# Optimization experiments

Measured on AMD Instinct MI355X. Metric: run time of the kernel, lower is better.

Reference implementation:

```python
import jax, jax.numpy as jnp
import numpy as np

D = 256   # feature_dim
NQ = 512  # num query keypoints
NK = 512  # num key/value keypoints


def setup_inputs() -> dict:
    key = jax.random.key(0)
    ks = jax.random.split(key, 10)
    def w(k, shape, fan_in):
        return jax.random.normal(k, shape, dtype=jnp.float32) / np.sqrt(fan_in)
    inp = {
        "x": jax.random.normal(ks[0], (1, D, NQ), dtype=jnp.float32),
        "source": jax.random.normal(ks[1], (1, D, NK), dtype=jnp.float32),
        # MLPAttention score MLP: Conv1d(2D->D,k=1), ReLU, Conv1d(D->1,k=1)
        "w1": w(ks[2], (D, 2 * D), 2 * D),
        "b1": w(ks[3], (D,), 2 * D),
        "w2": w(ks[4], (1, D), D),
        "b2": w(ks[5], (1,), D),
        # outer MLP: Conv1d(2D->2D,k=1), ReLU, Conv1d(2D->D,k=1) with zero bias init
        "wa": w(ks[6], (2 * D, 2 * D), 2 * D),
        "ba": w(ks[7], (2 * D,), 2 * D),
        "wb": w(ks[8], (D, 2 * D), 2 * D),
        "bb": jnp.zeros((D,), dtype=jnp.float32),
    }
    return inp


def reference(x, source, w1, b1, w2, b2, wa, ba, wb, bb):
    d = x.shape[1]
    q = x[0]       # [D, nq]
    k = source[0]  # [D, nk]
    # cat((q broadcast over nk, k broadcast over nq)) then Conv1d(2D->D) is
    # equivalent to splitting w1 into query/key halves and broadcasting:
    w1q, w1k = w1[:, :d], w1[:, d:]
    aq = w1q @ q + b1[:, None]                       # [D, nq]
    ak = w1k @ k                                     # [D, nk]
    h = jax.nn.relu(aq[:, :, None] + ak[:, None, :])  # [D, nq, nk]
    scores = (jnp.einsum('d,dnm->nm', w2[0], h) + b2[0])[None]  # [1, nq, nk]
    prob = jax.nn.softmax(scores, axis=-1)
    message = jnp.einsum('bnm,bdm->bdn', prob, source)  # [1, D, nq]
    # outer MLP on cat([x, message], channel dim)
    cat = jnp.concatenate([x, message], axis=1)         # [1, 2D, nq]
    h2 = jax.nn.relu(jnp.einsum('oc,bcn->bon', wa, cat) + ba[None, :, None])
    y = jnp.einsum('oc,bcn->bon', wb, h2) + bb[None, :, None]  # [1, D, nq]
    return (y, scores)
```

## Files before the change

### kernel.cpp

```cpp
#include <hip/hip_runtime.h>
#include <hip/hip_bf16.h>

#define DD 256
#define NN 512

typedef __attribute__((ext_vector_type(8))) short short8;
typedef __attribute__((ext_vector_type(4))) float floatx4;

__device__ __forceinline__ unsigned short f2bf(float f) {
  unsigned u = __float_as_uint(f);
  u += 0x7FFFu + ((u >> 16) & 1u);
  return (unsigned short)(u >> 16);
}

__device__ __forceinline__ short8 ldfrag(const unsigned short* __restrict__ base,
                                         int row, int ld, int k, int lane) {
  const unsigned short* p = base + (row + (lane & 15)) * ld + k + ((lane >> 4) << 3);
  return *(const short8*)p;
}

__device__ __forceinline__ void gemm_acc(floatx4 acc[4],
    const unsigned short* __restrict__ A, int lda,
    const unsigned short* __restrict__ BT, int ldb,
    int K, int a_k0, int b_k0, int m0, int n0, int lane) {
  for (int k = 0; k < K; k += 32) {
    short8 a = ldfrag(A, m0, lda, a_k0 + k, lane);
#pragma unroll
    for (int nf = 0; nf < 4; ++nf) {
      short8 b = ldfrag(BT, n0 + nf * 16, ldb, b_k0 + k, lane);
      acc[nf] = __builtin_amdgcn_mfma_f32_16x16x32_bf16(a, b, acc[nf], 0, 0, 0);
    }
  }
}

template <bool COLBIAS, bool ROWBIAS, bool RELU, bool OUTBF>
__device__ __forceinline__ void gemm_epi(floatx4 acc[4],
    const float* __restrict__ bias, void* __restrict__ C, int ldc,
    int m0, int n0, int lane) {
  const int col = lane & 15;
  const int q = lane >> 4;
#pragma unroll
  for (int nf = 0; nf < 4; ++nf) {
    const int n = n0 + nf * 16 + col;
    const float cb = COLBIAS ? bias[n] : 0.0f;
#pragma unroll
    for (int r = 0; r < 4; ++r) {
      const int m = m0 + q * 4 + r;
      float v = acc[nf][r] + cb + (ROWBIAS ? bias[m] : 0.0f);
      if (RELU) v = fmaxf(v, 0.0f);
      if (OUTBF) ((unsigned short*)C)[m * ldc + n] = f2bf(v);
      else       ((float*)C)[m * ldc + n] = v;
    }
  }
}

__device__ __forceinline__ void acc_zero(floatx4 acc[4]) {
#pragma unroll
  for (int i = 0; i < 4; ++i) {
    acc[i][0] = 0.f; acc[i][1] = 0.f; acc[i][2] = 0.f; acc[i][3] = 0.f;
  }
}

__global__ __launch_bounds__(256) void prep_kernel(
    const float* __restrict__ x, const float* __restrict__ src,
    const float* __restrict__ w1, const float* __restrict__ wa,
    const float* __restrict__ wb,
    unsigned short* __restrict__ w1b, unsigned short* __restrict__ wab,
    unsigned short* __restrict__ wbb, unsigned short* __restrict__ srcb,
    unsigned short* __restrict__ xT, unsigned short* __restrict__ srcT) {
  const int bid = blockIdx.x;
  const int tid = threadIdx.x;
  if (bid < 640) {
    const float* in; unsigned short* out; int off;
    if (bid < 128)      { in = w1;  out = w1b; off = bid; }
    else if (bid < 384) { in = wa;  out = wab; off = bid - 128; }
    else if (bid < 512) { in = wb;  out = wbb; off = bid - 384; }
    else                { in = src; out = srcb; off = bid - 512; }
    const int i = off * 1024 + tid * 4;
    const float4 v = *(const float4*)(in + i);
    const unsigned lo = (unsigned)f2bf(v.x) | ((unsigned)f2bf(v.y) << 16);
    const unsigned hi = (unsigned)f2bf(v.z) | ((unsigned)f2bf(v.w) << 16);
    *(uint2*)(out + i) = make_uint2(lo, hi);
  } else {
    __shared__ float tile[32][33];
    const int b = bid - 640;
    const float* in = (b >> 7) ? src : x;
    unsigned short* out = (b >> 7) ? srcT : xT;
    const int t = b & 127;
    const int n0 = (t >> 3) * 32;
    const int d0 = (t & 7) * 32;
    const int tx = tid & 31, ty = tid >> 5;
#pragma unroll
    for (int i = ty; i < 32; i += 8)
      tile[i][tx] = in[(d0 + i) * NN + n0 + tx];
    __syncthreads();
#pragma unroll
    for (int i = ty; i < 32; i += 8)
      out[(n0 + i) * DD + d0 + tx] = f2bf(tile[tx][i]);
  }
}

__global__ __launch_bounds__(64) void aqak_kernel(
    const unsigned short* __restrict__ xT, const unsigned short* __restrict__ srcT,
    const unsigned short* __restrict__ w1b, const float* __restrict__ b1,
    float* __restrict__ aqT, float* __restrict__ akT) {
  const int lane = threadIdx.x;
  const int m0 = blockIdx.y * 16;
  const int n0 = blockIdx.x * 64;
  floatx4 acc[4]; acc_zero(acc);
  if (blockIdx.z == 0) {
    gemm_acc(acc, xT, 256, w1b, 512, 256, 0, 0, m0, n0, lane);
    gemm_epi<true, false, false, false>(acc, b1, aqT, 256, m0, n0, lane);
  } else {
    gemm_acc(acc, srcT, 256, w1b + 256, 512, 256, 0, 0, m0, n0, lane);
    gemm_epi<false, false, false, false>(acc, nullptr, akT, 256, m0, n0, lane);
  }
}

__global__ __launch_bounds__(256) void scores_kernel(
    const float* __restrict__ aqT, const float* __restrict__ akT,
    const float* __restrict__ w2, const float* __restrict__ b2,
    float* __restrict__ sc) {
  const int tid = threadIdx.x;
  const int m = blockIdx.x * 32 + (tid & 31);
  const int n0t = blockIdx.y * 32 + (tid >> 5) * 4;
  const float* akp = akT + m * DD;
  const float* aq0 = aqT + n0t * DD;
  float s0 = 0.f, s1 = 0.f, s2 = 0.f, s3 = 0.f;
  for (int d = 0; d < DD; d += 4) {
    const float4 w = *(const float4*)(w2 + d);
    const float4 kv = *(const float4*)(akp + d);
    const float4 a0 = *(const float4*)(aq0 + d);
    const float4 a1 = *(const float4*)(aq0 + DD + d);
    const float4 a2 = *(const float4*)(aq0 + 2 * DD + d);
    const float4 a3 = *(const float4*)(aq0 + 3 * DD + d);
    s0 += w.x * fmaxf(a0.x + kv.x, 0.f) + w.y * fmaxf(a0.y + kv.y, 0.f)
        + w.z * fmaxf(a0.z + kv.z, 0.f) + w.w * fmaxf(a0.w + kv.w, 0.f);
    s1 += w.x * fmaxf(a1.x + kv.x, 0.f) + w.y * fmaxf(a1.y + kv.y, 0.f)
        + w.z * fmaxf(a1.z + kv.z, 0.f) + w.w * fmaxf(a1.w + kv.w, 0.f);
    s2 += w.x * fmaxf(a2.x + kv.x, 0.f) + w.y * fmaxf(a2.y + kv.y, 0.f)
        + w.z * fmaxf(a2.z + kv.z, 0.f) + w.w * fmaxf(a2.w + kv.w, 0.f);
    s3 += w.x * fmaxf(a3.x + kv.x, 0.f) + w.y * fmaxf(a3.y + kv.y, 0.f)
        + w.z * fmaxf(a3.z + kv.z, 0.f) + w.w * fmaxf(a3.w + kv.w, 0.f);
  }
  const float bv = b2[0];
  sc[(n0t + 0) * NN + m] = s0 + bv;
  sc[(n0t + 1) * NN + m] = s1 + bv;
  sc[(n0t + 2) * NN + m] = s2 + bv;
  sc[(n0t + 3) * NN + m] = s3 + bv;
}

__global__ __launch_bounds__(256) void softmax_kernel(
    const float* __restrict__ sc, unsigned short* __restrict__ probb) {
  __shared__ float red[256];
  const int n = blockIdx.x;
  const int t = threadIdx.x;
  const float v0 = sc[n * NN + t];
  const float v1 = sc[n * NN + 256 + t];
  red[t] = fmaxf(v0, v1);
  __syncthreads();
  for (int s = 128; s > 0; s >>= 1) {
    if (t < s) red[t] = fmaxf(red[t], red[t + s]);
    __syncthreads();
  }
  const float mx = red[0];
  __syncthreads();
  const float e0 = __expf(v0 - mx);
  const float e1 = __expf(v1 - mx);
  red[t] = e0 + e1;
  __syncthreads();
  for (int s = 128; s > 0; s >>= 1) {
    if (t < s) red[t] += red[t + s];
    __syncthreads();
  }
  const float inv = 1.0f / red[0];
  probb[n * NN + t]       = f2bf(e0 * inv);
  probb[n * NN + 256 + t] = f2bf(e1 * inv);
}

__global__ __launch_bounds__(64) void msgT_kernel(
    const unsigned short* __restrict__ probb, const unsigned short* __restrict__ srcb,
    unsigned short* __restrict__ msgTb) {
  const int lane = threadIdx.x;
  const int m0 = blockIdx.y * 16;
  const int n0 = blockIdx.x * 64;
  floatx4 acc[4]; acc_zero(acc);
  gemm_acc(acc, probb, 512, srcb, 512, 512, 0, 0, m0, n0, lane);
  gemm_epi<false, false, false, true>(acc, nullptr, msgTb, 256, m0, n0, lane);
}

__global__ __launch_bounds__(64) void h2T_kernel(
    const unsigned short* __restrict__ xT, const unsigned short* __restrict__ msgTb,
    const unsigned short* __restrict__ wab, const float* __restrict__ ba,
    unsigned short* __restrict__ h2Tb) {
  const int lane = threadIdx.x;
  const int m0 = blockIdx.y * 16;
  const int n0 = blockIdx.x * 64;
  floatx4 acc[4]; acc_zero(acc);
  gemm_acc(acc, xT,    256, wab, 512, 256, 0, 0,   m0, n0, lane);
  gemm_acc(acc, msgTb, 256, wab, 512, 256, 0, 256, m0, n0, lane);
  gemm_epi<true, false, true, true>(acc, ba, h2Tb, 512, m0, n0, lane);
}

__global__ __launch_bounds__(64) void y_kernel(
    const unsigned short* __restrict__ wbb, const unsigned short* __restrict__ h2Tb,
    const float* __restrict__ bb, float* __restrict__ y) {
  const int lane = threadIdx.x;
  const int m0 = blockIdx.y * 16;
  const int n0 = blockIdx.x * 64;
  floatx4 acc[4]; acc_zero(acc);
  gemm_acc(acc, wbb, 512, h2Tb, 512, 512, 0, 0, m0, n0, lane);
  gemm_epi<false, true, false, false>(acc, bb, y, 512, m0, n0, lane);
}

extern "C" void kernel_launch(void* const* d_in, const int* in_sizes, int n_in,
                              void* d_out, int out_size, void* d_ws, size_t ws_size,
                              hipStream_t stream) {
  (void)in_sizes; (void)n_in; (void)out_size; (void)ws_size;

  const float* x   = (const float*)d_in[0];
  const float* src = (const float*)d_in[1];
  const float* w1  = (const float*)d_in[2];
  const float* b1  = (const float*)d_in[3];
  const float* w2  = (const float*)d_in[4];
  const float* b2  = (const float*)d_in[5];
  const float* wa  = (const float*)d_in[6];
  const float* ba  = (const float*)d_in[7];
  const float* wb  = (const float*)d_in[8];
  const float* bb  = (const float*)d_in[9];

  float* y_out  = (float*)d_out;
  float* sc_out = (float*)d_out + 131072;

  char* ws = (char*)d_ws;
  unsigned short* w1b   = (unsigned short*)(ws);
  unsigned short* wab   = (unsigned short*)(ws + (256 << 10));
  unsigned short* wbb   = (unsigned short*)(ws + (768 << 10));
  unsigned short* srcb  = (unsigned short*)(ws + (1024 << 10));
  unsigned short* xT    = (unsigned short*)(ws + (1280 << 10));
  unsigned short* srcT  = (unsigned short*)(ws + (1536 << 10));
  unsigned short* probb = (unsigned short*)(ws + (1792 << 10));
  unsigned short* msgTb = (unsigned short*)(ws + (2304 << 10));
  unsigned short* h2Tb  = (unsigned short*)(ws + (2560 << 10));
  float*          aqT   = (float*)(ws + (3072 << 10));
  float*          akT   = (float*)(ws + (3584 << 10));

  prep_kernel<<<896, 256, 0, stream>>>(x, src, w1, wa, wb,
                                       w1b, wab, wbb, srcb, xT, srcT);
  aqak_kernel<<<dim3(4, 32, 2), 64, 0, stream>>>(xT, srcT, w1b, b1, aqT, akT);
  scores_kernel<<<dim3(16, 16), 256, 0, stream>>>(aqT, akT, w2, b2, sc_out);
  softmax_kernel<<<512, 256, 0, stream>>>(sc_out, probb);
  msgT_kernel<<<dim3(4, 32), 64, 0, stream>>>(probb, srcb, msgTb);
  h2T_kernel<<<dim3(8, 32), 64, 0, stream>>>(xT, msgTb, wab, ba, h2Tb);
  y_kernel<<<dim3(8, 16), 64, 0, stream>>>(wbb, h2Tb, bb, y_out);
}
```

Measured before the change: 117.5 us.

## Split-K GEMMs across four waves, fuse softmax into message GEMM, tile scores in LDS

Every MFMA GEMM kernel now runs four waves per block. Each wave handles a quarter of the K dimension, and the partial sums are combined through shared memory, so each block does less serial K-loop work. The softmax kernel is folded into the message GEMM: each block recomputes row max, sum and bf16 probabilities for its 16 rows into LDS, which removes one launch and the prob buffer round trip. The softmax is redundantly repeated for each of the 4 column blocks. The aq/ak GEMM is re-laid out to a D-major [D,N] layout so the scores kernel can stage aq/ak tiles in shared memory and write float4 outputs, at the cost of extra LDS traffic and barriers.

```diff
diff --git a/kernel.cpp b/kernel.cpp
--- a/kernel.cpp
+++ b/kernel.cpp
@@ -12,17 +12,19 @@
   u += 0x7FFFu + ((u >> 16) & 1u);
   return (unsigned short)(u >> 16);
 }
+__device__ __forceinline__ unsigned pack2(float a, float b) {
+  return (unsigned)f2bf(a) | ((unsigned)f2bf(b) << 16);
+}
 
 __device__ __forceinline__ short8 ldfrag(const unsigned short* __restrict__ base,
                                          int row, int ld, int k, int lane) {
-  const unsigned short* p = base + (row + (lane & 15)) * ld + k + ((lane >> 4) << 3);
-  return *(const short8*)p;
+  return *(const short8*)(base + (row + (lane & 15)) * ld + k + ((lane >> 4) << 3));
 }
 
 __device__ __forceinline__ void gemm_acc(floatx4 acc[4],
-    const unsigned short* __restrict__ A, int lda,
-    const unsigned short* __restrict__ BT, int ldb,
-    int K, int a_k0, int b_k0, int m0, int n0, int lane) {
+    const unsigned short* __restrict__ A, int lda, int a_k0,
+    const unsigned short* __restrict__ BT, int ldb, int b_k0,
+    int K, int m0, int n0, int lane) {
   for (int k = 0; k < K; k += 32) {
     short8 a = ldfrag(A, m0, lda, a_k0 + k, lane);
 #pragma unroll
@@ -30,6 +32,37 @@
       short8 b = ldfrag(BT, n0 + nf * 16, ldb, b_k0 + k, lane);
       acc[nf] = __builtin_amdgcn_mfma_f32_16x16x32_bf16(a, b, acc[nf], 0, 0, 0);
     }
+  }
+}
+
+__device__ __forceinline__ void acc_zero(floatx4 acc[4]) {
+#pragma unroll
+  for (int i = 0; i < 4; ++i) {
+    acc[i][0] = 0.f; acc[i][1] = 0.f; acc[i][2] = 0.f; acc[i][3] = 0.f;
+  }
+}
+
+__device__ __forceinline__ void ksplit_combine(floatx4 acc[4], float* red,
+                                               int wave, int lane) {
+  const int col = lane & 15;
+  const int q = lane >> 4;
+  if (wave > 0) {
+    float* base = red + (wave - 1) * 1024;
+#pragma unroll
+    for (int nf = 0; nf < 4; ++nf)
+#pragma unroll
+      for (int r = 0; r < 4; ++r)
+        base[(q * 4 + r) * 64 + nf * 16 + col] = acc[nf][r];
+  }
+  __syncthreads();
+  if (wave == 0) {
+#pragma unroll
+    for (int nf = 0; nf < 4; ++nf)
+#pragma unroll
+      for (int r = 0; r < 4; ++r) {
+        const int idx = (q * 4 + r) * 64 + nf * 16 + col;
+        acc[nf][r] += red[idx] + red[1024 + idx] + red[2048 + idx];
+      }
   }
 }
 
@@ -51,13 +84,6 @@
       if (OUTBF) ((unsigned short*)C)[m * ldc + n] = f2bf(v);
       else       ((float*)C)[m * ldc + n] = v;
     }
-  }
-}
-
-__device__ __forceinline__ void acc_zero(floatx4 acc[4]) {
-#pragma unroll
-  for (int i = 0; i < 4; ++i) {
-    acc[i][0] = 0.f; acc[i][1] = 0.f; acc[i][2] = 0.f; acc[i][3] = 0.f;
   }
 }
 
@@ -78,9 +104,7 @@
     else                { in = src; out = srcb; off = bid - 512; }
     const int i = off * 1024 + tid * 4;
     const float4 v = *(const float4*)(in + i);
-    const unsigned lo = (unsigned)f2bf(v.x) | ((unsigned)f2bf(v.y) << 16);
-    const unsigned hi = (unsigned)f2bf(v.z) | ((unsigned)f2bf(v.w) << 16);
-    *(uint2*)(out + i) = make_uint2(lo, hi);
+    *(uint2*)(out + i) = make_uint2(pack2(v.x, v.y), pack2(v.z, v.w));
   } else {
     __shared__ float tile[32][33];
     const int b = bid - 640;
@@ -100,117 +124,186 @@
   }
 }
 
-__global__ __launch_bounds__(64) void aqak_kernel(
+__global__ __launch_bounds__(256) void aqak_kernel(
     const unsigned short* __restrict__ xT, const unsigned short* __restrict__ srcT,
     const unsigned short* __restrict__ w1b, const float* __restrict__ b1,
-    float* __restrict__ aqT, float* __restrict__ akT) {
-  const int lane = threadIdx.x;
+    float* __restrict__ aq, float* __restrict__ ak) {
+  __shared__ float red[3072];
+  const int tid = threadIdx.x;
+  const int lane = tid & 63;
+  const int wave = tid >> 6;
   const int m0 = blockIdx.y * 16;
   const int n0 = blockIdx.x * 64;
+  const int z = blockIdx.z;
+  const unsigned short* BT = z ? srcT : xT;
+
   floatx4 acc[4]; acc_zero(acc);
-  if (blockIdx.z == 0) {
-    gemm_acc(acc, xT, 256, w1b, 512, 256, 0, 0, m0, n0, lane);
-    gemm_epi<true, false, false, false>(acc, b1, aqT, 256, m0, n0, lane);
-  } else {
-    gemm_acc(acc, srcT, 256, w1b + 256, 512, 256, 0, 0, m0, n0, lane);
-    gemm_epi<false, false, false, false>(acc, nullptr, akT, 256, m0, n0, lane);
+  gemm_acc(acc, w1b, NN, z * 256 + wave * 64, BT, DD, wave * 64, 64, m0, n0, lane);
+  ksplit_combine(acc, red, wave, lane);
+  if (wave == 0) {
+    if (z == 0) gemm_epi<false, true, false, false>(acc, b1, aq, NN, m0, n0, lane);
+    else        gemm_epi<false, false, false, false>(acc, nullptr, ak, NN, m0, n0, lane);
   }
 }
 
 __global__ __launch_bounds__(256) void scores_kernel(
-    const float* __restrict__ aqT, const float* __restrict__ akT,
+    const float* __restrict__ aq, const float* __restrict__ ak,
     const float* __restrict__ w2, const float* __restrict__ b2,
     float* __restrict__ sc) {
-  const int tid = threadIdx.x;
-  const int m = blockIdx.x * 32 + (tid & 31);
-  const int n0t = blockIdx.y * 32 + (tid >> 5) * 4;
-  const float* akp = akT + m * DD;
-  const float* aq0 = aqT + n0t * DD;
+  __shared__ float aqs[128][32];
+  __shared__ float aks[128][32];
+  __shared__ float w2s[DD];
+
+  const int tid = threadIdx.x;
+  const int n0 = blockIdx.x * 32;
+  const int m0 = blockIdx.y * 32;
+  const int tn = tid & 31;
+  const int tm4 = (tid >> 5) * 4;
+
+  w2s[tid] = w2[tid];
+
   float s0 = 0.f, s1 = 0.f, s2 = 0.f, s3 = 0.f;
-  for (int d = 0; d < DD; d += 4) {
-    const float4 w = *(const float4*)(w2 + d);
-    const float4 kv = *(const float4*)(akp + d);
-    const float4 a0 = *(const float4*)(aq0 + d);
-    const float4 a1 = *(const float4*)(aq0 + DD + d);
-    const float4 a2 = *(const float4*)(aq0 + 2 * DD + d);
-    const float4 a3 = *(const float4*)(aq0 + 3 * DD + d);
-    s0 += w.x * fmaxf(a0.x + kv.x, 0.f) + w.y * fmaxf(a0.y + kv.y, 0.f)
-        + w.z * fmaxf(a0.z + kv.z, 0.f) + w.w * fmaxf(a0.w + kv.w, 0.f);
-    s1 += w.x * fmaxf(a1.x + kv.x, 0.f) + w.y * fmaxf(a1.y + kv.y, 0.f)
-        + w.z * fmaxf(a1.z + kv.z, 0.f) + w.w * fmaxf(a1.w + kv.w, 0.f);
-    s2 += w.x * fmaxf(a2.x + kv.x, 0.f) + w.y * fmaxf(a2.y + kv.y, 0.f)
-        + w.z * fmaxf(a2.z + kv.z, 0.f) + w.w * fmaxf(a2.w + kv.w, 0.f);
-    s3 += w.x * fmaxf(a3.x + kv.x, 0.f) + w.y * fmaxf(a3.y + kv.y, 0.f)
-        + w.z * fmaxf(a3.z + kv.z, 0.f) + w.w * fmaxf(a3.w + kv.w, 0.f);
-  }
+
+  for (int d0 = 0; d0 < DD; d0 += 128) {
+    __syncthreads();
+#pragma unroll
+    for (int k = 0; k < 16; ++k) {
+      const int idx = k * 256 + tid;
+      const int r = idx >> 5, cc = idx & 31;
+      aqs[r][cc] = aq[(d0 + r) * NN + n0 + cc];
+      aks[r][cc] = ak[(d0 + r) * NN + m0 + cc];
+    }
+    __syncthreads();
+
+    for (int dd = 0; dd < 128; ++dd) {
+      const float w = w2s[d0 + dd];
+      const float a = aqs[dd][tn];
+      const float4 akv = *(const float4*)&aks[dd][tm4];
+      s0 += w * fmaxf(a + akv.x, 0.f);
+      s1 += w * fmaxf(a + akv.y, 0.f);
+      s2 += w * fmaxf(a + akv.z, 0.f);
+      s3 += w * fmaxf(a + akv.w, 0.f);
+    }
+  }
+
   const float bv = b2[0];
-  sc[(n0t + 0) * NN + m] = s0 + bv;
-  sc[(n0t + 1) * NN + m] = s1 + bv;
-  sc[(n0t + 2) * NN + m] = s2 + bv;
-  sc[(n0t + 3) * NN + m] = s3 + bv;
-}
-
-__global__ __launch_bounds__(256) void softmax_kernel(
-    const float* __restrict__ sc, unsigned short* __restrict__ probb) {
-  __shared__ float red[256];
-  const int n = blockIdx.x;
-  const int t = threadIdx.x;
-  const float v0 = sc[n * NN + t];
-  const float v1 = sc[n * NN + 256 + t];
-  red[t] = fmaxf(v0, v1);
-  __syncthreads();
-  for (int s = 128; s > 0; s >>= 1) {
-    if (t < s) red[t] = fmaxf(red[t], red[t + s]);
-    __syncthreads();
-  }
-  const float mx = red[0];
-  __syncthreads();
-  const float e0 = __expf(v0 - mx);
-  const float e1 = __expf(v1 - mx);
-  red[t] = e0 + e1;
-  __syncthreads();
-  for (int s = 128; s > 0; s >>= 1) {
-    if (t < s) red[t] += red[t + s];
-    __syncthreads();
-  }
-  const float inv = 1.0f / red[0];
-  probb[n * NN + t]       = f2bf(e0 * inv);
-  probb[n * NN + 256 + t] = f2bf(e1 * inv);
-}
-
-__global__ __launch_bounds__(64) void msgT_kernel(
-    const unsigned short* __restrict__ probb, const unsigned short* __restrict__ srcb,
+  float4 o;
+  o.x = s0 + bv; o.y = s1 + bv; o.z = s2 + bv; o.w = s3 + bv;
+  *(float4*)&sc[(n0 + tn) * NN + m0 + tm4] = o;
+}
+
+__global__ __launch_bounds__(256) void msgT_kernel(
+    const float* __restrict__ sc, const unsigned short* __restrict__ srcb,
     unsigned short* __restrict__ msgTb) {
-  const int lane = threadIdx.x;
-  const int m0 = blockIdx.y * 16;
-  const int n0 = blockIdx.x * 64;
+  __shared__ unsigned short Ap[16][520];
+  __shared__ float red[3072];
+  __shared__ float smax[16][16];
+  __shared__ float ssum[16][16];
+  __shared__ float rst[16][2];
+
+  const int tid = threadIdx.x;
+  const int lane = tid & 63;
+  const int wave = tid >> 6;
+  const int n0 = blockIdx.y * 16;
+  const int d0 = blockIdx.x * 64;
+
+  const int r = tid >> 4;
+  const int seg = tid & 15;
+  float4 v[8];
+  const float* rp = sc + (n0 + r) * NN + seg * 32;
+#pragma unroll
+  for (int i = 0; i < 8; ++i) v[i] = *(const float4*)(rp + i * 4);
+
+  float mx = -3.0e38f;
+#pragma unroll
+  for (int i = 0; i < 8; ++i)
+    mx = fmaxf(mx, fmaxf(fmaxf(v[i].x, v[i].y), fmaxf(v[i].z, v[i].w)));
+  smax[r][seg] = mx;
+  __syncthreads();
+  if (seg == 0) {
+    float m2 = smax[r][0];
+#pragma unroll
+    for (int i = 1; i < 16; ++i) m2 = fmaxf(m2, smax[r][i]);
+    rst[r][0] = m2;
+  }
+  __syncthreads();
+  mx = rst[r][0];
+
+  float sum = 0.f;
+#pragma unroll
+  for (int i = 0; i < 8; ++i) {
+    v[i].x = __expf(v[i].x - mx); v[i].y = __expf(v[i].y - mx);
+    v[i].z = __expf(v[i].z - mx); v[i].w = __expf(v[i].w - mx);
+    sum += v[i].x + v[i].y + v[i].z + v[i].w;
+  }
+  ssum[r][seg] = sum;
+  __syncthreads();
+  if (seg == 0) {
+    float s2 = ssum[r][0];
+#pragma unroll
+    for (int i = 1; i < 16; ++i) s2 += ssum[r][i];
+    rst[r][1] = s2;
+  }
+  __syncthreads();
+  const float inv = 1.0f / rst[r][1];
+#pragma unroll
+  for (int i = 0; i < 8; ++i) {
+    *(unsigned*)&Ap[r][seg * 32 + i * 4]     = pack2(v[i].x * inv, v[i].y * inv);
+    *(unsigned*)&Ap[r][seg * 32 + i * 4 + 2] = pack2(v[i].z * inv, v[i].w * inv);
+  }
+  __syncthreads();
+
   floatx4 acc[4]; acc_zero(acc);
-  gemm_acc(acc, probb, 512, srcb, 512, 512, 0, 0, m0, n0, lane);
-  gemm_epi<false, false, false, true>(acc, nullptr, msgTb, 256, m0, n0, lane);
-}
-
-__global__ __launch_bounds__(64) void h2T_kernel(
+  const int k0w = wave * 128;
+  const int arow = lane & 15;
+  const int koff = (lane >> 4) << 3;
+  for (int k = 0; k < 128; k += 32) {
+    short8 a = *(const short8*)&Ap[arow][k0w + k + koff];
+#pragma unroll
+    for (int nf = 0; nf < 4; ++nf) {
+      short8 b = ldfrag(srcb, d0 + nf * 16, NN, k0w + k, lane);
+      acc[nf] = __builtin_amdgcn_mfma_f32_16x16x32_bf16(a, b, acc[nf], 0, 0, 0);
+    }
+  }
+  ksplit_combine(acc, red, wave, lane);
+  if (wave == 0)
+    gemm_epi<false, false, false, true>(acc, nullptr, msgTb, DD, n0, d0, lane);
+}
+
+__global__ __launch_bounds__(256) void h2T_kernel(
     const unsigned short* __restrict__ xT, const unsigned short* __restrict__ msgTb,
     const unsigned short* __restrict__ wab, const float* __restrict__ ba,
     unsigned short* __restrict__ h2Tb) {
-  const int lane = threadIdx.x;
+  __shared__ float red[3072];
+  const int tid = threadIdx.x;
+  const int lane = tid & 63;
+  const int wave = tid >> 6;
   const int m0 = blockIdx.y * 16;
   const int n0 = blockIdx.x * 64;
+
   floatx4 acc[4]; acc_zero(acc);
-  gemm_acc(acc, xT,    256, wab, 512, 256, 0, 0,   m0, n0, lane);
-  gemm_acc(acc, msgTb, 256, wab, 512, 256, 0, 256, m0, n0, lane);
-  gemm_epi<true, false, true, true>(acc, ba, h2Tb, 512, m0, n0, lane);
-}
-
-__global__ __launch_bounds__(64) void y_kernel(
+  const unsigned short* A = (wave < 2) ? xT : msgTb;
+  gemm_acc(acc, A, DD, (wave & 1) * 128, wab, NN, wave * 128, 128, m0, n0, lane);
+  ksplit_combine(acc, red, wave, lane);
+  if (wave == 0)
+    gemm_epi<true, false, true, true>(acc, ba, h2Tb, NN, m0, n0, lane);
+}
+
+__global__ __launch_bounds__(256) void y_kernel(
     const unsigned short* __restrict__ wbb, const unsigned short* __restrict__ h2Tb,
     const float* __restrict__ bb, float* __restrict__ y) {
-  const int lane = threadIdx.x;
+  __shared__ float red[3072];
+  const int tid = threadIdx.x;
+  const int lane = tid & 63;
+  const int wave = tid >> 6;
   const int m0 = blockIdx.y * 16;
   const int n0 = blockIdx.x * 64;
+
   floatx4 acc[4]; acc_zero(acc);
-  gemm_acc(acc, wbb, 512, h2Tb, 512, 512, 0, 0, m0, n0, lane);
-  gemm_epi<false, true, false, false>(acc, bb, y, 512, m0, n0, lane);
+  gemm_acc(acc, wbb, NN, wave * 128, h2Tb, NN, wave * 128, 128, m0, n0, lane);
+  ksplit_combine(acc, red, wave, lane);
+  if (wave == 0)
+    gemm_epi<false, true, false, false>(acc, bb, y, NN, m0, n0, lane);
 }
 
 extern "C" void kernel_launch(void* const* d_in, const int* in_sizes, int n_in,
@@ -239,18 +332,16 @@
   unsigned short* srcb  = (unsigned short*)(ws + (1024 << 10));
   unsigned short* xT    = (unsigned short*)(ws + (1280 << 10));
   unsigned short* srcT  = (unsigned short*)(ws + (1536 << 10));
-  unsigned short* probb = (unsigned short*)(ws + (1792 << 10));
-  unsigned short* msgTb = (unsigned short*)(ws + (2304 << 10));
-  unsigned short* h2Tb  = (unsigned short*)(ws + (2560 << 10));
-  float*          aqT   = (float*)(ws + (3072 << 10));
-  float*          akT   = (float*)(ws + (3584 << 10));
+  unsigned short* msgTb = (unsigned short*)(ws + (1792 << 10));
+  unsigned short* h2Tb  = (unsigned short*)(ws + (2048 << 10));
+  float*          aq    = (float*)(ws + (2560 << 10));
+  float*          ak    = (float*)(ws + (3072 << 10));
 
   prep_kernel<<<896, 256, 0, stream>>>(x, src, w1, wa, wb,
                                        w1b, wab, wbb, srcb, xT, srcT);
-  aqak_kernel<<<dim3(4, 32, 2), 64, 0, stream>>>(xT, srcT, w1b, b1, aqT, akT);
-  scores_kernel<<<dim3(16, 16), 256, 0, stream>>>(aqT, akT, w2, b2, sc_out);
-  softmax_kernel<<<512, 256, 0, stream>>>(sc_out, probb);
-  msgT_kernel<<<dim3(4, 32), 64, 0, stream>>>(probb, srcb, msgTb);
-  h2T_kernel<<<dim3(8, 32), 64, 0, stream>>>(xT, msgTb, wab, ba, h2Tb);
-  y_kernel<<<dim3(8, 16), 64, 0, stream>>>(wbb, h2Tb, bb, y_out);
-}
+  aqak_kernel<<<dim3(8, 16, 2), 256, 0, stream>>>(xT, srcT, w1b, b1, aq, ak);
+  scores_kernel<<<dim3(16, 16), 256, 0, stream>>>(aq, ak, w2, b2, sc_out);
+  msgT_kernel<<<dim3(4, 32), 256, 0, stream>>>(sc_out, srcb, msgTb);
+  h2T_kernel<<<dim3(8, 32), 256, 0, stream>>>(xT, msgTb, wab, ba, h2Tb);
+  y_kernel<<<dim3(8, 16), 256, 0, stream>>>(wbb, h2Tb, bb, y_out);
+}
```

After: 108.4 us. 1.08x faster.
